# Performance work log

Hardware: AMD Instinct MI355X
Metric: run time of the kernel (lower is better)

Reference implementation:

```python
import jax, jax.numpy as jnp
import numpy as np

IN_FEATURES = 512
OUT_FEATURES = 256
N = 2048

def setup_inputs() -> dict:
    key = jax.random.key(0)
    k1, k2, k3 = jax.random.split(key, 3)
    x = jax.random.normal(k1, (N, IN_FEATURES), dtype=jnp.float32)
    # kaiming_uniform_(a=sqrt(5)) -> uniform(-b, b) with b = sqrt(6/((1+5)*fan_in)) = 1/sqrt(fan_in)
    bound_w = 1.0 / np.sqrt(IN_FEATURES)
    weight = jax.random.uniform(k2, (OUT_FEATURES, IN_FEATURES), dtype=jnp.float32,
                                minval=-bound_w, maxval=bound_w)
    bound_b = 1.0 / np.sqrt(IN_FEATURES)
    bias = jax.random.uniform(k3, (OUT_FEATURES,), dtype=jnp.float32,
                              minval=-bound_b, maxval=bound_b)
    return {"x": x, "weight": weight, "bias": bias}

def reference(x, weight, bias):
    # MAM fully-connected (beta == 0 path):
    # prod[n, k, j] = x[n, k] * weight[j, k]
    # C[n, j] = max_k prod[n,k,j] + min_k prod[n,k,j] + bias[j]
    prod = x[:, :, None] * weight.T[None, :, :]   # [N, in, out]
    C = jnp.max(prod, axis=1) + jnp.min(prod, axis=1) + bias[None, :]
    return C
```

## Files before the change

kernel.cpp:

```cpp
#include <hip/hip_runtime.h>
#include <math.h>

#define N_ 2048
#define K_ 512
#define J_ 256
#define SPLIT 8
#define KR  (K_ / SPLIT)
#define KR4 (KR / 4)

typedef __attribute__((ext_vector_type(2))) float v2f;

__global__ __launch_bounds__(256, 4) void mam_partial(
    const float* __restrict__ x, const float* __restrict__ w,
    float* __restrict__ pmax, float* __restrict__ pmin)
{
    __shared__ __align__(16) float xs[64 * 64];
    __shared__ __align__(16) float wsh[64 * 64];

    const int t  = threadIdx.x;
    const int tx = t & 15;
    const int ty = t >> 4;
    const int n0 = blockIdx.x * 64;
    const int j0 = blockIdx.y * 64;
    const int kc = blockIdx.z * KR;

#pragma unroll
    for (int r = 0; r < 4; ++r) {
        const int idx = r * 256 + t;
        const int row = idx >> 4;
        const int kq  = idx & 15;
        const int c   = (kq + (row >> 2)) & 15;
        const float4 gx = *(const float4*)(x + (size_t)(n0 + row) * K_ + kc + kq * 4);
        *(float4*)&xs[row * 64 + c * 4] = gx;
        const float4 gw = *(const float4*)(w + (size_t)(j0 + row) * K_ + kc + kq * 4);
        *(float4*)&wsh[row * 64 + c * 4] = gw;
    }
    __syncthreads();

    float mx[4][4], mn[4][4];
#pragma unroll
    for (int i = 0; i < 4; ++i)
#pragma unroll
        for (int j = 0; j < 4; ++j) { mx[i][j] = -__builtin_inff(); mn[i][j] = __builtin_inff(); }

#pragma unroll 4
    for (int k4 = 0; k4 < KR4; ++k4) {
        float4 xv[4], wv[4];
#pragma unroll
        for (int i = 0; i < 4; ++i)
            xv[i] = *(const float4*)&xs[(ty * 4 + i) * 64 + (((k4 + ty) & 15) * 4)];
#pragma unroll
        for (int j = 0; j < 4; ++j)
            wv[j] = *(const float4*)&wsh[(tx * 4 + j) * 64 + (((k4 + tx) & 15) * 4)];
#pragma unroll
        for (int i = 0; i < 4; ++i) {
            const v2f xa = {xv[i].x, xv[i].y};
            const v2f xb = {xv[i].z, xv[i].w};
#pragma unroll
            for (int j = 0; j < 4; ++j) {
                const v2f wa = {wv[j].x, wv[j].y};
                const v2f wb = {wv[j].z, wv[j].w};
                const v2f pA = xa * wa;
                const v2f pB = xb * wb;
                mx[i][j] = fmaxf(fmaxf(mx[i][j], pA.x), pA.y);
                mn[i][j] = fminf(fminf(mn[i][j], pA.x), pA.y);
                mx[i][j] = fmaxf(fmaxf(mx[i][j], pB.x), pB.y);
                mn[i][j] = fminf(fminf(mn[i][j], pB.x), pB.y);
            }
        }
    }

    const size_t base = ((size_t)blockIdx.z * N_ + n0 + ty * 4) * J_ + j0 + tx * 4;
#pragma unroll
    for (int i = 0; i < 4; ++i) {
        *(float4*)(pmax + base + (size_t)i * J_) = make_float4(mx[i][0], mx[i][1], mx[i][2], mx[i][3]);
        *(float4*)(pmin + base + (size_t)i * J_) = make_float4(mn[i][0], mn[i][1], mn[i][2], mn[i][3]);
    }
}

__global__ __launch_bounds__(256) void mam_combine(
    const float* __restrict__ pmax, const float* __restrict__ pmin,
    const float* __restrict__ bias, float* __restrict__ out)
{
    const int f = blockIdx.x * 256 + threadIdx.x;
    const int PLANE4 = N_ * J_ / 4;
    const float4* pm = (const float4*)pmax;
    const float4* pn = (const float4*)pmin;

    float4 a = pm[f];
    float4 b = pn[f];
#pragma unroll
    for (int s = 1; s < SPLIT; ++s) {
        const float4 a2 = pm[(size_t)s * PLANE4 + f];
        const float4 b2 = pn[(size_t)s * PLANE4 + f];
        a.x = fmaxf(a.x, a2.x); a.y = fmaxf(a.y, a2.y);
        a.z = fmaxf(a.z, a2.z); a.w = fmaxf(a.w, a2.w);
        b.x = fminf(b.x, b2.x); b.y = fminf(b.y, b2.y);
        b.z = fminf(b.z, b2.z); b.w = fminf(b.w, b2.w);
    }
    const float4 bi = ((const float4*)bias)[f & (J_ / 4 - 1)];
    float4 o;
    o.x = a.x + b.x + bi.x;
    o.y = a.y + b.y + bi.y;
    o.z = a.z + b.z + bi.z;
    o.w = a.w + b.w + bi.w;
    ((float4*)out)[f] = o;
}

__global__ __launch_bounds__(256) void mam_naive(
    const float* __restrict__ x, const float* __restrict__ w,
    const float* __restrict__ bias, float* __restrict__ out)
{
    const int n = blockIdx.x;
    const int j = threadIdx.x;
    float mx = -__builtin_inff(), mn = __builtin_inff();
    for (int k = 0; k < K_; ++k) {
        const float p = x[(size_t)n * K_ + k] * w[(size_t)j * K_ + k];
        mx = fmaxf(mx, p);
        mn = fminf(mn, p);
    }
    out[(size_t)n * J_ + j] = mx + mn + bias[j];
}

extern "C" void kernel_launch(void* const* d_in, const int* in_sizes, int n_in,
                              void* d_out, int out_size, void* d_ws, size_t ws_size,
                              hipStream_t stream) {
    const float* x    = (const float*)d_in[0];
    const float* w    = (const float*)d_in[1];
    const float* bias = (const float*)d_in[2];
    float* out = (float*)d_out;

    const size_t need = (size_t)SPLIT * 2 * N_ * J_ * sizeof(float);
    if (ws_size >= need) {
        float* pmax = (float*)d_ws;
        float* pmin = pmax + (size_t)SPLIT * N_ * J_;
        dim3 grid(N_ / 64, J_ / 64, SPLIT);
        mam_partial<<<grid, 256, 0, stream>>>(x, w, pmax, pmin);
        mam_combine<<<(N_ * J_ / 4) / 256, 256, 0, stream>>>(pmax, pmin, bias, out);
    } else {
        mam_naive<<<N_, 256, 0, stream>>>(x, w, bias, out);
    }
}
```

Baseline: 84.57 us.

## Retile partial kernel to 32x256 blocks with full-J weight slab in LDS

The partial kernel now gives each block 32 rows of x and all 256 output columns for one K split, so the weight slab for that split is loaded once per block. Each thread accumulates a 4x8 tile instead of 4x4, which raises arithmetic per LDS read, and the grid shrinks to 512 one-dimensional blocks. The combine kernel's block-to-row mapping is rearranged to match the tile order. LDS use grows to about 72KB per block and register pressure rises, so occupancy drops (launch bounds lowered to 2), and the smaller grid may underfill the GPU.

```diff
diff --git a/kernel.cpp b/kernel.cpp
--- a/kernel.cpp
+++ b/kernel.cpp
@@ -10,71 +10,86 @@
 
 typedef __attribute__((ext_vector_type(2))) float v2f;
 
-__global__ __launch_bounds__(256, 4) void mam_partial(
+__global__ __launch_bounds__(256, 2) void mam_partial(
     const float* __restrict__ x, const float* __restrict__ w,
     float* __restrict__ pmax, float* __restrict__ pmin)
 {
-    __shared__ __align__(16) float xs[64 * 64];
-    __shared__ __align__(16) float wsh[64 * 64];
+    __shared__ __align__(16) float4 xs[32 * 16];
+    __shared__ __align__(16) float4 wsh[256 * 16];
 
-    const int t  = threadIdx.x;
-    const int tx = t & 15;
-    const int ty = t >> 4;
-    const int n0 = blockIdx.x * 64;
-    const int j0 = blockIdx.y * 64;
-    const int kc = blockIdx.z * KR;
+    const int t     = threadIdx.x;
+    const int id    = blockIdx.x;
+    const int tile  = id & 63;
+    const int split = id >> 6;
+    const int n0    = tile * 32;
+    const int kc    = split * KR;
+
+    const int lane = t & 63;
+    const int wave = t >> 6;
+    const int lj   = lane & 7;
+    const int ln   = lane >> 3;
+    const int jbase = wave * 64 + lj * 8;
 
 #pragma unroll
-    for (int r = 0; r < 4; ++r) {
+    for (int r = 0; r < 2; ++r) {
         const int idx = r * 256 + t;
         const int row = idx >> 4;
-        const int kq  = idx & 15;
-        const int c   = (kq + (row >> 2)) & 15;
-        const float4 gx = *(const float4*)(x + (size_t)(n0 + row) * K_ + kc + kq * 4);
-        *(float4*)&xs[row * 64 + c * 4] = gx;
-        const float4 gw = *(const float4*)(w + (size_t)(j0 + row) * K_ + kc + kq * 4);
-        *(float4*)&wsh[row * 64 + c * 4] = gw;
+        const int q   = idx & 15;
+        const float4 g = *(const float4*)(x + (size_t)(n0 + row) * K_ + kc + q * 4);
+        xs[row * 16 + ((q + (row >> 2)) & 15)] = g;
+    }
+#pragma unroll
+    for (int r = 0; r < 16; ++r) {
+        const int idx = r * 256 + t;
+        const int jr  = idx >> 4;
+        const int q   = idx & 15;
+        const float4 g = *(const float4*)(w + (size_t)jr * K_ + kc + q * 4);
+        wsh[jr * 16 + ((q + (jr >> 3)) & 15)] = g;
     }
     __syncthreads();
 
-    float mx[4][4], mn[4][4];
+    float mx[4][8], mn[4][8];
 #pragma unroll
     for (int i = 0; i < 4; ++i)
 #pragma unroll
-        for (int j = 0; j < 4; ++j) { mx[i][j] = -__builtin_inff(); mn[i][j] = __builtin_inff(); }
+        for (int j = 0; j < 8; ++j) { mx[i][j] = -__builtin_inff(); mn[i][j] = __builtin_inff(); }
 
-#pragma unroll 4
+    const int wrow = jbase >> 3;
+#pragma unroll 2
     for (int k4 = 0; k4 < KR4; ++k4) {
-        float4 xv[4], wv[4];
+        float4 xv[4], wv[8];
 #pragma unroll
         for (int i = 0; i < 4; ++i)
-            xv[i] = *(const float4*)&xs[(ty * 4 + i) * 64 + (((k4 + ty) & 15) * 4)];
+            xv[i] = xs[(ln * 4 + i) * 16 + ((k4 + ln) & 15)];
+        const int cw = (k4 + wrow) & 15;
 #pragma unroll
-        for (int j = 0; j < 4; ++j)
-            wv[j] = *(const float4*)&wsh[(tx * 4 + j) * 64 + (((k4 + tx) & 15) * 4)];
+        for (int jj = 0; jj < 8; ++jj)
+            wv[jj] = wsh[(jbase + jj) * 16 + cw];
 #pragma unroll
         for (int i = 0; i < 4; ++i) {
             const v2f xa = {xv[i].x, xv[i].y};
             const v2f xb = {xv[i].z, xv[i].w};
 #pragma unroll
-            for (int j = 0; j < 4; ++j) {
-                const v2f wa = {wv[j].x, wv[j].y};
-                const v2f wb = {wv[j].z, wv[j].w};
+            for (int jj = 0; jj < 8; ++jj) {
+                const v2f wa = {wv[jj].x, wv[jj].y};
+                const v2f wb = {wv[jj].z, wv[jj].w};
                 const v2f pA = xa * wa;
                 const v2f pB = xb * wb;
-                mx[i][j] = fmaxf(fmaxf(mx[i][j], pA.x), pA.y);
-                mn[i][j] = fminf(fminf(mn[i][j], pA.x), pA.y);
-                mx[i][j] = fmaxf(fmaxf(mx[i][j], pB.x), pB.y);
-                mn[i][j] = fminf(fminf(mn[i][j], pB.x), pB.y);
+                mx[i][jj] = fmaxf(fmaxf(mx[i][jj], pA.x), pA.y);
+                mn[i][jj] = fminf(fminf(mn[i][jj], pA.x), pA.y);
+                mx[i][jj] = fmaxf(fmaxf(mx[i][jj], pB.x), pB.y);
+                mn[i][jj] = fminf(fminf(mn[i][jj], pB.x), pB.y);
             }
         }
     }
 
-    const size_t base = ((size_t)blockIdx.z * N_ + n0 + ty * 4) * J_ + j0 + tx * 4;
 #pragma unroll
     for (int i = 0; i < 4; ++i) {
-        *(float4*)(pmax + base + (size_t)i * J_) = make_float4(mx[i][0], mx[i][1], mx[i][2], mx[i][3]);
-        *(float4*)(pmin + base + (size_t)i * J_) = make_float4(mn[i][0], mn[i][1], mn[i][2], mn[i][3]);
+        const size_t off = ((size_t)split * N_ + n0 + ln * 4 + i) * J_ + jbase;
+        *(float4*)(pmax + off)     = make_float4(mx[i][0], mx[i][1], mx[i][2], mx[i][3]);
+        *(float4*)(pmax + off + 4) = make_float4(mx[i][4], mx[i][5], mx[i][6], mx[i][7]);
+        *(float4*)(pmin + off)     = make_float4(mn[i][0], mn[i][1], mn[i][2], mn[i][3]);
+        *(float4*)(pmin + off + 4) = make_float4(mn[i][4], mn[i][5], mn[i][6], mn[i][7]);
     }
 }
 
@@ -82,28 +97,35 @@
     const float* __restrict__ pmax, const float* __restrict__ pmin,
     const float* __restrict__ bias, float* __restrict__ out)
 {
-    const int f = blockIdx.x * 256 + threadIdx.x;
+    const int b    = blockIdx.x;
+    const int tile = b & 63;
+    const int sub  = b >> 6;
+    const int tid  = threadIdx.x;
+    const int r    = tid >> 6;
+    const int col4 = tid & 63;
+    const int n    = tile * 32 + sub * 4 + r;
+    const int f    = n * (J_ / 4) + col4;
     const int PLANE4 = N_ * J_ / 4;
+
     const float4* pm = (const float4*)pmax;
     const float4* pn = (const float4*)pmin;
-
     float4 a = pm[f];
-    float4 b = pn[f];
+    float4 c = pn[f];
 #pragma unroll
     for (int s = 1; s < SPLIT; ++s) {
         const float4 a2 = pm[(size_t)s * PLANE4 + f];
-        const float4 b2 = pn[(size_t)s * PLANE4 + f];
+        const float4 c2 = pn[(size_t)s * PLANE4 + f];
         a.x = fmaxf(a.x, a2.x); a.y = fmaxf(a.y, a2.y);
         a.z = fmaxf(a.z, a2.z); a.w = fmaxf(a.w, a2.w);
-        b.x = fminf(b.x, b2.x); b.y = fminf(b.y, b2.y);
-        b.z = fminf(b.z, b2.z); b.w = fminf(b.w, b2.w);
+        c.x = fminf(c.x, c2.x); c.y = fminf(c.y, c2.y);
+        c.z = fminf(c.z, c2.z); c.w = fminf(c.w, c2.w);
     }
-    const float4 bi = ((const float4*)bias)[f & (J_ / 4 - 1)];
+    const float4 bi = ((const float4*)bias)[col4];
     float4 o;
-    o.x = a.x + b.x + bi.x;
-    o.y = a.y + b.y + bi.y;
-    o.z = a.z + b.z + bi.z;
-    o.w = a.w + b.w + bi.w;
+    o.x = a.x + c.x + bi.x;
+    o.y = a.y + c.y + bi.y;
+    o.z = a.z + c.z + bi.z;
+    o.w = a.w + c.w + bi.w;
     ((float4*)out)[f] = o;
 }
 
@@ -134,9 +156,8 @@
     if (ws_size >= need) {
         float* pmax = (float*)d_ws;
         float* pmin = pmax + (size_t)SPLIT * N_ * J_;
-        dim3 grid(N_ / 64, J_ / 64, SPLIT);
-        mam_partial<<<grid, 256, 0, stream>>>(x, w, pmax, pmin);
-        mam_combine<<<(N_ * J_ / 4) / 256, 256, 0, stream>>>(pmax, pmin, bias, out);
+        mam_partial<<<dim3(64 * SPLIT), 256, 0, stream>>>(x, w, pmax, pmin);
+        mam_combine<<<dim3(512), 256, 0, stream>>>(pmax, pmin, bias, out);
     } else {
         mam_naive<<<N_, 256, 0, stream>>>(x, w, bias, out);
     }
```

New measurement: 88.74 us. 4.9% more time.

## Restructure partial kernel to register-resident weights with per-thread output column

Applied to the files above, without the earlier changes.

Replaces the LDS-tiled 64x64 register-blocked partial kernel with a scheme where each thread keeps a 32-wide K slice of one weight row in registers and streams 16 x rows, computing one output per row. The K split grows from 8 to 16, and x rows are double-buffered through wave-uniform loads instead of shared memory. This removes LDS traffic and the barrier, but doubles the partial-result workspace written and read by the combine kernel and lowers data reuse per thread. The combine kernel is remapped to match the new launch.

```diff
diff --git a/kernel.cpp b/kernel.cpp
--- a/kernel.cpp
+++ b/kernel.cpp
@@ -4,9 +4,9 @@
 #define N_ 2048
 #define K_ 512
 #define J_ 256
-#define SPLIT 8
-#define KR  (K_ / SPLIT)
-#define KR4 (KR / 4)
+#define KS 16
+#define KSL (K_ / KS)
+#define NB 16
 
 typedef __attribute__((ext_vector_type(2))) float v2f;
 
@@ -14,96 +14,88 @@
     const float* __restrict__ x, const float* __restrict__ w,
     float* __restrict__ pmax, float* __restrict__ pmin)
 {
-    __shared__ __align__(16) float xs[64 * 64];
-    __shared__ __align__(16) float wsh[64 * 64];
+    const int t  = threadIdx.x;
+    const int nb = blockIdx.x;
+    const int ks = blockIdx.y;
+    const int n0 = nb * NB;
+    const int kc = ks * KSL;
 
-    const int t  = threadIdx.x;
-    const int tx = t & 15;
-    const int ty = t >> 4;
-    const int n0 = blockIdx.x * 64;
-    const int j0 = blockIdx.y * 64;
-    const int kc = blockIdx.z * KR;
+    float4 wr[8];
+    const float4* wp = (const float4*)(w + (size_t)t * K_ + kc);
+#pragma unroll
+    for (int q = 0; q < 8; ++q) wr[q] = wp[q];
 
+    const float* xp = x + (size_t)n0 * K_ + kc;
+
+    float4 xa[8], xb[8];
 #pragma unroll
-    for (int r = 0; r < 4; ++r) {
-        const int idx = r * 256 + t;
-        const int row = idx >> 4;
-        const int kq  = idx & 15;
-        const int c   = (kq + (row >> 2)) & 15;
-        const float4 gx = *(const float4*)(x + (size_t)(n0 + row) * K_ + kc + kq * 4);
-        *(float4*)&xs[row * 64 + c * 4] = gx;
-        const float4 gw = *(const float4*)(w + (size_t)(j0 + row) * K_ + kc + kq * 4);
-        *(float4*)&wsh[row * 64 + c * 4] = gw;
-    }
-    __syncthreads();
+    for (int q = 0; q < 8; ++q) xa[q] = ((const float4*)xp)[q];
 
-    float mx[4][4], mn[4][4];
-#pragma unroll
-    for (int i = 0; i < 4; ++i)
-#pragma unroll
-        for (int j = 0; j < 4; ++j) { mx[i][j] = -__builtin_inff(); mn[i][j] = __builtin_inff(); }
-
-#pragma unroll 4
-    for (int k4 = 0; k4 < KR4; ++k4) {
-        float4 xv[4], wv[4];
-#pragma unroll
-        for (int i = 0; i < 4; ++i)
-            xv[i] = *(const float4*)&xs[(ty * 4 + i) * 64 + (((k4 + ty) & 15) * 4)];
-#pragma unroll
-        for (int j = 0; j < 4; ++j)
-            wv[j] = *(const float4*)&wsh[(tx * 4 + j) * 64 + (((k4 + tx) & 15) * 4)];
-#pragma unroll
-        for (int i = 0; i < 4; ++i) {
-            const v2f xa = {xv[i].x, xv[i].y};
-            const v2f xb = {xv[i].z, xv[i].w};
-#pragma unroll
-            for (int j = 0; j < 4; ++j) {
-                const v2f wa = {wv[j].x, wv[j].y};
-                const v2f wb = {wv[j].z, wv[j].w};
-                const v2f pA = xa * wa;
-                const v2f pB = xb * wb;
-                mx[i][j] = fmaxf(fmaxf(mx[i][j], pA.x), pA.y);
-                mn[i][j] = fminf(fminf(mn[i][j], pA.x), pA.y);
-                mx[i][j] = fmaxf(fmaxf(mx[i][j], pB.x), pB.y);
-                mn[i][j] = fminf(fminf(mn[i][j], pB.x), pB.y);
-            }
-        }
+#define REDUCE_STORE(BUF, NIDX)                                            \
+    {                                                                      \
+        float mx = -__builtin_inff(), mn = __builtin_inff();               \
+        _Pragma("unroll")                                                  \
+        for (int q = 0; q < 8; ++q) {                                      \
+            const v2f pa = (v2f){BUF[q].x, BUF[q].y} *                     \
+                           (v2f){wr[q].x, wr[q].y};                        \
+            const v2f pb = (v2f){BUF[q].z, BUF[q].w} *                     \
+                           (v2f){wr[q].z, wr[q].w};                        \
+            mx = fmaxf(fmaxf(mx, pa.x), pa.y);                             \
+            mn = fminf(fminf(mn, pa.x), pa.y);                             \
+            mx = fmaxf(fmaxf(mx, pb.x), pb.y);                             \
+            mn = fminf(fminf(mn, pb.x), pb.y);                             \
+        }                                                                  \
+        const size_t off = ((size_t)ks * N_ + n0 + (NIDX)) * J_ + t;       \
+        pmax[off] = mx;                                                    \
+        pmin[off] = mn;                                                    \
     }
 
-    const size_t base = ((size_t)blockIdx.z * N_ + n0 + ty * 4) * J_ + j0 + tx * 4;
+    for (int n = 0; n < NB; n += 2) {
+        const float* p1 = xp + (size_t)(n + 1) * K_;
 #pragma unroll
-    for (int i = 0; i < 4; ++i) {
-        *(float4*)(pmax + base + (size_t)i * J_) = make_float4(mx[i][0], mx[i][1], mx[i][2], mx[i][3]);
-        *(float4*)(pmin + base + (size_t)i * J_) = make_float4(mn[i][0], mn[i][1], mn[i][2], mn[i][3]);
+        for (int q = 0; q < 8; ++q) xb[q] = ((const float4*)p1)[q];
+        REDUCE_STORE(xa, n)
+        if (n + 2 < NB) {
+            const float* p2 = xp + (size_t)(n + 2) * K_;
+#pragma unroll
+            for (int q = 0; q < 8; ++q) xa[q] = ((const float4*)p2)[q];
+        }
+        REDUCE_STORE(xb, n + 1)
     }
+#undef REDUCE_STORE
 }
 
 __global__ __launch_bounds__(256) void mam_combine(
     const float* __restrict__ pmax, const float* __restrict__ pmin,
     const float* __restrict__ bias, float* __restrict__ out)
 {
-    const int f = blockIdx.x * 256 + threadIdx.x;
+    const int b   = blockIdx.x;
+    const int nb  = b & 127;
+    const int sub = b >> 7;
+    const int n   = nb * NB + sub * 4 + (threadIdx.x >> 6);
+    const int c4  = threadIdx.x & 63;
+    const int f   = n * (J_ / 4) + c4;
     const int PLANE4 = N_ * J_ / 4;
+
     const float4* pm = (const float4*)pmax;
     const float4* pn = (const float4*)pmin;
-
     float4 a = pm[f];
-    float4 b = pn[f];
+    float4 c = pn[f];
 #pragma unroll
-    for (int s = 1; s < SPLIT; ++s) {
+    for (int s = 1; s < KS; ++s) {
         const float4 a2 = pm[(size_t)s * PLANE4 + f];
-        const float4 b2 = pn[(size_t)s * PLANE4 + f];
+        const float4 c2 = pn[(size_t)s * PLANE4 + f];
         a.x = fmaxf(a.x, a2.x); a.y = fmaxf(a.y, a2.y);
         a.z = fmaxf(a.z, a2.z); a.w = fmaxf(a.w, a2.w);
-        b.x = fminf(b.x, b2.x); b.y = fminf(b.y, b2.y);
-        b.z = fminf(b.z, b2.z); b.w = fminf(b.w, b2.w);
+        c.x = fminf(c.x, c2.x); c.y = fminf(c.y, c2.y);
+        c.z = fminf(c.z, c2.z); c.w = fminf(c.w, c2.w);
     }
-    const float4 bi = ((const float4*)bias)[f & (J_ / 4 - 1)];
+    const float4 bi = ((const float4*)bias)[c4];
     float4 o;
-    o.x = a.x + b.x + bi.x;
-    o.y = a.y + b.y + bi.y;
-    o.z = a.z + b.z + bi.z;
-    o.w = a.w + b.w + bi.w;
+    o.x = a.x + c.x + bi.x;
+    o.y = a.y + c.y + bi.y;
+    o.z = a.z + c.z + bi.z;
+    o.w = a.w + c.w + bi.w;
     ((float4*)out)[f] = o;
 }
 
@@ -130,13 +122,12 @@
     const float* bias = (const float*)d_in[2];
     float* out = (float*)d_out;
 
-    const size_t need = (size_t)SPLIT * 2 * N_ * J_ * sizeof(float);
+    const size_t need = (size_t)KS * 2 * N_ * J_ * sizeof(float);
     if (ws_size >= need) {
         float* pmax = (float*)d_ws;
-        float* pmin = pmax + (size_t)SPLIT * N_ * J_;
-        dim3 grid(N_ / 64, J_ / 64, SPLIT);
-        mam_partial<<<grid, 256, 0, stream>>>(x, w, pmax, pmin);
-        mam_combine<<<(N_ * J_ / 4) / 256, 256, 0, stream>>>(pmax, pmin, bias, out);
+        float* pmin = pmax + (size_t)KS * N_ * J_;
+        mam_partial<<<dim3(N_ / NB, KS), 256, 0, stream>>>(x, w, pmax, pmin);
+        mam_combine<<<dim3(512), 256, 0, stream>>>(pmax, pmin, bias, out);
     } else {
         mam_naive<<<N_, 256, 0, stream>>>(x, w, bias, out);
     }
```

Measured after the change: 93.56 us. 10.6% more time.
